# Kernel tuning notes

Measured on AMD Instinct MI355X. Metric: run time of the kernel, lower is better.

Reference implementation:

```python
import jax, jax.numpy as jnp
import numpy as np

N = 50000      # nodes
E = 500000     # edges
F_IN = 128     # num_features
H = 128        # hidden_dim
G = 256        # graphs in batch


def setup_inputs() -> dict:
    key = jax.random.key(0)
    ks = jax.random.split(key, 12)
    x = jax.random.normal(ks[0], (N, F_IN), jnp.float32)
    edge_index = jax.random.randint(ks[1], (2, E), 0, N, dtype=jnp.int32)
    edge_attr = jax.random.uniform(ks[2], (E,), jnp.float32)  # positive edge weights
    batch = jnp.sort(jax.random.randint(ks[3], (N,), 0, G, dtype=jnp.int32))
    s_in = 1.0 / np.sqrt(F_IN)
    s_h = 1.0 / np.sqrt(H)
    return {
        "x": x,
        "edge_index": edge_index,
        "edge_attr": edge_attr,
        "batch": batch,
        "W1": jax.random.normal(ks[4], (H, F_IN), jnp.float32) * s_in,
        "b1": jnp.zeros((H,), jnp.float32),
        "W2": jax.random.normal(ks[5], (H, H), jnp.float32) * s_h,
        "b2": jnp.zeros((H,), jnp.float32),
        "fW1": jax.random.normal(ks[6], (H, H), jnp.float32) * s_h,
        "fb1": jnp.zeros((H,), jnp.float32),
        "fW2": jax.random.normal(ks[7], (1, H), jnp.float32) * s_h,
        "fb2": jnp.zeros((1,), jnp.float32),
    }


def gcn_conv(x, src, dst, ew, W, b, n):
    """PyG GCNConv: linear transform, add self-loops (weight 1),
    symmetric deg^-1/2 normalization with edge weights, scatter-add, bias."""
    h = x @ W.T                                   # [n, H]
    loop = jnp.arange(n, dtype=src.dtype)
    s = jnp.concatenate([src, loop])
    d = jnp.concatenate([dst, loop])
    w = jnp.concatenate([ew, jnp.ones((n,), x.dtype)])
    deg = jax.ops.segment_sum(w, d, num_segments=n)  # weighted in-degree incl. self-loop
    dinv = jnp.where(deg > 0, jax.lax.rsqrt(deg), 0.0)
    norm = dinv[s] * w * dinv[d]                  # [E+n]
    msg = h[s] * norm[:, None]                    # gather + scale: [E+n, H]
    out = jax.ops.segment_sum(msg, d, num_segments=n)  # scatter-add
    return out + b


def reference(x, edge_index, edge_attr, batch, W1, b1, W2, b2, fW1, fb1, fW2, fb2):
    src, dst = edge_index[0], edge_index[1]
    h = jax.nn.relu(gcn_conv(x, src, dst, edge_attr, W1, b1, N))
    h = jax.nn.relu(gcn_conv(h, src, dst, edge_attr, W2, b2, N))
    # global_mean_pool over graph ids
    sums = jax.ops.segment_sum(h, batch, num_segments=G)            # [G, H]
    counts = jax.ops.segment_sum(jnp.ones((N,), h.dtype), batch, num_segments=G)
    pooled = sums / jnp.maximum(counts, 1.0)[:, None]
    o = jax.nn.relu(pooled @ fW1.T + fb1)
    return o @ fW2.T + fb2                                          # [G, 1]
```

## Files before the change

kernel.cpp:

```cpp
#include <hip/hip_runtime.h>
#include <hip/hip_bf16.h>


#define CAP 32
#define STRIDE 64

typedef __attribute__((ext_vector_type(8))) short short8;
typedef __attribute__((ext_vector_type(4))) float floatx4;

__device__ inline unsigned short f2bf(float f) {
    unsigned int u = __float_as_uint(f);
    u += 0x7FFF + ((u >> 16) & 1);
    return (unsigned short)(u >> 16);
}
__device__ inline float bf2f(unsigned short h) {
    return __uint_as_float(((unsigned int)h) << 16);
}

__global__ void build_csr(const int* __restrict__ src, const int* __restrict__ dst,
                          const float* __restrict__ ew,
                          int* __restrict__ cnt, int2* __restrict__ csr, int e, int n) {
    int i = blockIdx.x * blockDim.x + threadIdx.x;
    if (i < e) {
        int d = dst[i];
        int r = i & 1;
        int pos = atomicAdd(&cnt[(size_t)r * n + d], 1);
        csr[((size_t)d << 6) + (r << 5) + pos] = make_int2(src[i], __float_as_int(ew[i]));
    }
}

__global__ __launch_bounds__(256) void deg_from_csr(const int* __restrict__ cnt,
        const int2* __restrict__ csr, float* __restrict__ dinv, int n) {
    int node = blockIdx.x * 8 + (threadIdx.x >> 5);
    int lane = threadIdx.x & 31;
    float s = 0.0f;
    if (node < n) {
        int c0 = cnt[node], c1 = cnt[n + node];
        const int2* b = csr + ((size_t)node << 6);
        if (lane < c0) s += __int_as_float(b[lane].y);
        if (lane < c1) s += __int_as_float(b[CAP + lane].y);
    }
#pragma unroll
    for (int off = 16; off > 0; off >>= 1) s += __shfl_down(s, off, 32);
    if (node < n && lane == 0) dinv[node] = rsqrtf(s + 1.0f);
}

__global__ __launch_bounds__(256) void fold_dinv(const int* __restrict__ cnt,
        int2* __restrict__ csr, const float* __restrict__ dinv, int n) {
    int node = blockIdx.x * 8 + (threadIdx.x >> 5);
    if (node >= n) return;
    int lane = threadIdx.x & 31;
    int c0 = cnt[node], c1 = cnt[n + node];
    int2* b = csr + ((size_t)node << 6);
    if (lane < c0) {
        int2 e = b[lane];
        e.y = __float_as_int(__int_as_float(e.y) * dinv[e.x]);
        b[lane] = e;
    }
    if (lane < c1) {
        int2 e = b[CAP + lane];
        e.y = __float_as_int(__int_as_float(e.y) * dinv[e.x]);
        b[CAP + lane] = e;
    }
}

#define PW 136
__global__ __launch_bounds__(256) void gemm_nt_mfma(const float* __restrict__ X,
        const float* __restrict__ W, unsigned short* __restrict__ C, int M) {
    __shared__ unsigned short whi[128 * PW];
    __shared__ unsigned short wlo[128 * PW];
    const int t = threadIdx.x;

    {
        int j = t >> 1;
        int c0 = (t & 1) * 64;
        const floatx4* wr = (const floatx4*)(W + (size_t)j * 128 + c0);
        unsigned short* dh = &whi[j * PW + c0];
        unsigned short* dl = &wlo[j * PW + c0];
#pragma unroll
        for (int i = 0; i < 16; ++i) {
            floatx4 v = wr[i];
            ushort4 hv, lv;
            hv.x = f2bf(v.x); lv.x = f2bf(v.x - bf2f(hv.x));
            hv.y = f2bf(v.y); lv.y = f2bf(v.y - bf2f(hv.y));
            hv.z = f2bf(v.z); lv.z = f2bf(v.z - bf2f(hv.z));
            hv.w = f2bf(v.w); lv.w = f2bf(v.w - bf2f(hv.w));
            *(ushort4*)(dh + i * 4) = hv;
            *(ushort4*)(dl + i * 4) = lv;
        }
    }
    __syncthreads();

    const int wave = t >> 6;
    const int lane = t & 63;
    const int q = lane >> 4;
    const int ln = lane & 15;
    const int rowbase = blockIdx.x * 128 + wave * 32;

    floatx4 acc[2][8];
#pragma unroll
    for (int s = 0; s < 2; ++s)
#pragma unroll
        for (int ct = 0; ct < 8; ++ct) acc[s][ct] = (floatx4){0.f, 0.f, 0.f, 0.f};

#pragma unroll
    for (int ks = 0; ks < 4; ++ks) {
        short8 ahi[2], alo[2];
#pragma unroll
        for (int s = 0; s < 2; ++s) {
            int row = rowbase + s * 16 + ln;
            int rowc = (row < M) ? row : (M - 1);
            const floatx4* xr = (const floatx4*)(X + (size_t)rowc * 128 + ks * 32 + q * 8);
            floatx4 x0 = xr[0];
            floatx4 x1 = xr[1];
            unsigned short h, l;
            h = f2bf(x0.x); l = f2bf(x0.x - bf2f(h)); ahi[s][0] = (short)h; alo[s][0] = (short)l;
            h = f2bf(x0.y); l = f2bf(x0.y - bf2f(h)); ahi[s][1] = (short)h; alo[s][1] = (short)l;
            h = f2bf(x0.z); l = f2bf(x0.z - bf2f(h)); ahi[s][2] = (short)h; alo[s][2] = (short)l;
            h = f2bf(x0.w); l = f2bf(x0.w - bf2f(h)); ahi[s][3] = (short)h; alo[s][3] = (short)l;
            h = f2bf(x1.x); l = f2bf(x1.x - bf2f(h)); ahi[s][4] = (short)h; alo[s][4] = (short)l;
            h = f2bf(x1.y); l = f2bf(x1.y - bf2f(h)); ahi[s][5] = (short)h; alo[s][5] = (short)l;
            h = f2bf(x1.z); l = f2bf(x1.z - bf2f(h)); ahi[s][6] = (short)h; alo[s][6] = (short)l;
            h = f2bf(x1.w); l = f2bf(x1.w - bf2f(h)); ahi[s][7] = (short)h; alo[s][7] = (short)l;
        }
#pragma unroll
        for (int ct = 0; ct < 8; ++ct) {
            int lidx = (ct * 16 + ln) * PW + ks * 32 + q * 8;
            short8 bhi = *(const short8*)&whi[lidx];
            short8 blo = *(const short8*)&wlo[lidx];
#pragma unroll
            for (int s = 0; s < 2; ++s) {
                acc[s][ct] = __builtin_amdgcn_mfma_f32_16x16x32_bf16(ahi[s], bhi, acc[s][ct], 0, 0, 0);
                acc[s][ct] = __builtin_amdgcn_mfma_f32_16x16x32_bf16(ahi[s], blo, acc[s][ct], 0, 0, 0);
                acc[s][ct] = __builtin_amdgcn_mfma_f32_16x16x32_bf16(alo[s], bhi, acc[s][ct], 0, 0, 0);
            }
        }
    }

#pragma unroll
    for (int s = 0; s < 2; ++s) {
#pragma unroll
        for (int r = 0; r < 4; ++r) {
            int row = rowbase + s * 16 + q * 4 + r;
            if (row < M) {
                unsigned short* cr = C + (size_t)row * 128 + ln;
#pragma unroll
                for (int ct = 0; ct < 8; ++ct) cr[ct * 16] = f2bf(acc[s][ct][r]);
            }
        }
    }
}

__global__ __launch_bounds__(256) void aggregate_finalize(
        const unsigned short* __restrict__ h, const unsigned short* __restrict__ hlin,
        const int* __restrict__ cnt, const int2* __restrict__ csr,
        const float* __restrict__ dinv, const float* __restrict__ bias,
        float* __restrict__ outb, int n) {
    int node = blockIdx.x * 8 + (threadIdx.x >> 5);
    if (node >= n) return;
    int lane = threadIdx.x & 31;
    float di = dinv[node];
    float sl = di * di;
    float4 b4 = ((const float4*)bias)[lane];
    ushort4 bse = ((const ushort4*)(hlin + (size_t)node * 128))[lane];
    float4 acc = make_float4(0.f, 0.f, 0.f, 0.f);

    const int2* b = csr + ((size_t)node << 6);
    int c0 = cnt[node], c1 = cnt[n + node];
#pragma unroll
    for (int seg = 0; seg < 2; ++seg) {
        const int2* bs = b + seg * CAP;
        int c = seg ? c1 : c0;
        const int4* bv = (const int4*)bs;
        int k = 0;
        for (; k + 2 <= c; k += 2) {
            int4 e2 = bv[k >> 1];
            float w0 = __int_as_float(e2.y);
            float w1 = __int_as_float(e2.w);
            ushort4 h0 = ((const ushort4*)(h + (size_t)e2.x * 128))[lane];
            ushort4 h1 = ((const ushort4*)(h + (size_t)e2.z * 128))[lane];
            acc.x += bf2f(h0.x) * w0 + bf2f(h1.x) * w1;
            acc.y += bf2f(h0.y) * w0 + bf2f(h1.y) * w1;
            acc.z += bf2f(h0.z) * w0 + bf2f(h1.z) * w1;
            acc.w += bf2f(h0.w) * w0 + bf2f(h1.w) * w1;
        }
        if (k < c) {
            int2 ed = bs[k];
            float w = __int_as_float(ed.y);
            ushort4 hv = ((const ushort4*)(h + (size_t)ed.x * 128))[lane];
            acc.x += bf2f(hv.x) * w;
            acc.y += bf2f(hv.y) * w;
            acc.z += bf2f(hv.z) * w;
            acc.w += bf2f(hv.w) * w;
        }
    }
    float4 o;
    o.x = fmaxf(acc.x * di + bf2f(bse.x) * sl + b4.x, 0.0f);
    o.y = fmaxf(acc.y * di + bf2f(bse.y) * sl + b4.y, 0.0f);
    o.z = fmaxf(acc.z * di + bf2f(bse.z) * sl + b4.z, 0.0f);
    o.w = fmaxf(acc.w * di + bf2f(bse.w) * sl + b4.w, 0.0f);
    ((float4*)(outb + (size_t)node * 128))[lane] = o;
}

#define POOL_BLOCKS 1024
__global__ __launch_bounds__(128) void pool_partial(const float* __restrict__ h,
        const int* __restrict__ batch, float* __restrict__ pooled, int n) {
    int chunk = (n + POOL_BLOCKS - 1) / POOL_BLOCKS;
    int s = blockIdx.x * chunk;
    if (s >= n) return;
    int e = min(s + chunk, n);
    int j = threadIdx.x;
    int curg = batch[s];
    float sum = 0.0f;
    for (int i = s; i < e; ++i) {
        int g = batch[i];
        if (g != curg) {
            atomicAdd(&pooled[(size_t)curg * 128 + j], sum);
            sum = 0.0f;
            curg = g;
        }
        sum += h[(size_t)i * 128 + j];
    }
    atomicAdd(&pooled[(size_t)curg * 128 + j], sum);
}

__global__ __launch_bounds__(128) void head_mlp(const float* __restrict__ pooled,
        const int* __restrict__ batch, int n,
        const float* __restrict__ fW1, const float* __restrict__ fb1,
        const float* __restrict__ fW2, const float* __restrict__ fb2,
        float* __restrict__ out) {
    int g = blockIdx.x;
    int j = threadIdx.x;
    int lo = 0, hi = n;
    while (lo < hi) { int mid = (lo + hi) >> 1; if (batch[mid] < g) lo = mid + 1; else hi = mid; }
    int s = lo;
    hi = n;
    while (lo < hi) { int mid = (lo + hi) >> 1; if (batch[mid] < g + 1) lo = mid + 1; else hi = mid; }
    int cnt = lo - s;
    float scale = 1.0f / fmaxf((float)cnt, 1.0f);

    __shared__ float row[128];
    __shared__ float part[2];
    row[j] = pooled[(size_t)g * 128 + j] * scale;
    __syncthreads();
    float acc = fb1[j];
    const float* wr = fW1 + (size_t)j * 128;
#pragma unroll 8
    for (int k = 0; k < 128; ++k) acc += row[k] * wr[k];
    float v = fmaxf(acc, 0.0f) * fW2[j];
#pragma unroll
    for (int off = 32; off > 0; off >>= 1) v += __shfl_down(v, off);
    if ((j & 63) == 0) part[j >> 6] = v;
    __syncthreads();
    if (j == 0) out[g] = part[0] + part[1] + fb2[0];
}

extern "C" void kernel_launch(void* const* d_in, const int* in_sizes, int n_in,
                              void* d_out, int out_size, void* d_ws, size_t ws_size,
                              hipStream_t stream) {
    const float* x   = (const float*)d_in[0];
    const int*   ei  = (const int*)d_in[1];
    const float* ew  = (const float*)d_in[2];
    const int* batch = (const int*)d_in[3];
    const float* W1  = (const float*)d_in[4];
    const float* b1  = (const float*)d_in[5];
    const float* W2  = (const float*)d_in[6];
    const float* b2  = (const float*)d_in[7];
    const float* fW1 = (const float*)d_in[8];
    const float* fb1 = (const float*)d_in[9];
    const float* fW2 = (const float*)d_in[10];
    const float* fb2 = (const float*)d_in[11];
    float* out = (float*)d_out;

    const int N = in_sizes[0] / 128;
    const int E = in_sizes[2];
    const int G = out_size;
    const int* src = ei;
    const int* dst = ei + E;

    unsigned short* A = (unsigned short*)d_ws;
    float* B    = (float*)(A + (size_t)N * 128);
    int2*  csr  = (int2*)(B + (size_t)N * 128);
    int*   cnt  = (int*)(csr + (size_t)N * STRIDE);
    float* dinv = (float*)(cnt + (size_t)2 * N);
    float* pooled = dinv + N;

    hipMemsetAsync(cnt, 0, (size_t)2 * N * sizeof(int), stream);
    build_csr<<<(E + 255) / 256, 256, 0, stream>>>(src, dst, ew, cnt, csr, E, N);
    deg_from_csr<<<(N + 7) / 8, 256, 0, stream>>>(cnt, csr, dinv, N);
    fold_dinv<<<(N + 7) / 8, 256, 0, stream>>>(cnt, csr, dinv, N);

    gemm_nt_mfma<<<(N + 127) / 128, 256, 0, stream>>>(x, W1, A, N);
    aggregate_finalize<<<(N + 7) / 8, 256, 0, stream>>>(A, A, cnt, csr, dinv, b1, B, N);

    gemm_nt_mfma<<<(N + 127) / 128, 256, 0, stream>>>(B, W2, A, N);
    aggregate_finalize<<<(N + 7) / 8, 256, 0, stream>>>(A, A, cnt, csr, dinv, b2, B, N);

    hipMemsetAsync(pooled, 0, (size_t)G * 128 * sizeof(float), stream);
    pool_partial<<<POOL_BLOCKS, 128, 0, stream>>>(B, batch, pooled, N);
    head_mlp<<<G, 128, 0, stream>>>(pooled, batch, N, fW1, fb1, fW2, fb2, out);
}
```

Before: 244.8 us.

## Use four CSR count replicas, compact per-node edge lists, unroll aggregation by four

Edges are binned into four per-node sub-buckets of 16 slots instead of two of 32, which spreads the atomic counter traffic in CSR construction. The dinv-folding pass now also compacts the four sub-buckets into one contiguous list and writes the total count. The aggregation kernel then walks a single list with a 4-way unrolled gather, aiming for more loads in flight and less segment-loop overhead. The cost is extra index arithmetic in the fold pass, and each sub-bucket now overflows above 16 edges instead of 32.

```diff
diff --git a/kernel.cpp b/kernel.cpp
--- a/kernel.cpp
+++ b/kernel.cpp
@@ -2,7 +2,8 @@
 #include <hip/hip_bf16.h>
 
 
-#define CAP 32
+#define CAP 16
+#define NREP 4
 #define STRIDE 64
 
 typedef __attribute__((ext_vector_type(8))) short short8;
@@ -23,9 +24,9 @@
     int i = blockIdx.x * blockDim.x + threadIdx.x;
     if (i < e) {
         int d = dst[i];
-        int r = i & 1;
+        int r = i & (NREP - 1);
         int pos = atomicAdd(&cnt[(size_t)r * n + d], 1);
-        csr[((size_t)d << 6) + (r << 5) + pos] = make_int2(src[i], __float_as_int(ew[i]));
+        csr[((size_t)d << 6) + (r << 4) + pos] = make_int2(src[i], __float_as_int(ew[i]));
     }
 }
 
@@ -35,33 +36,45 @@
     int lane = threadIdx.x & 31;
     float s = 0.0f;
     if (node < n) {
-        int c0 = cnt[node], c1 = cnt[n + node];
+        int pos = lane & 15;
+        int sa = lane >> 4;
+        int sb = 2 + (lane >> 4);
+        int ca = cnt[(size_t)sa * n + node];
+        int cb = cnt[(size_t)sb * n + node];
         const int2* b = csr + ((size_t)node << 6);
-        if (lane < c0) s += __int_as_float(b[lane].y);
-        if (lane < c1) s += __int_as_float(b[CAP + lane].y);
+        if (pos < ca) s += __int_as_float(b[lane].y);
+        if (pos < cb) s += __int_as_float(b[32 + lane].y);
     }
 #pragma unroll
     for (int off = 16; off > 0; off >>= 1) s += __shfl_down(s, off, 32);
     if (node < n && lane == 0) dinv[node] = rsqrtf(s + 1.0f);
 }
 
-__global__ __launch_bounds__(256) void fold_dinv(const int* __restrict__ cnt,
+__global__ __launch_bounds__(256) void fold_compact(int* __restrict__ cnt,
         int2* __restrict__ csr, const float* __restrict__ dinv, int n) {
     int node = blockIdx.x * 8 + (threadIdx.x >> 5);
     if (node >= n) return;
     int lane = threadIdx.x & 31;
-    int c0 = cnt[node], c1 = cnt[n + node];
+    int c0 = cnt[node];
+    int c1 = cnt[(size_t)1 * n + node];
+    int c2 = cnt[(size_t)2 * n + node];
+    int c3 = cnt[(size_t)3 * n + node];
+    int pre[4] = {0, c0, c0 + c1, c0 + c1 + c2};
+    int cs[4] = {c0, c1, c2, c3};
+
     int2* b = csr + ((size_t)node << 6);
-    if (lane < c0) {
-        int2 e = b[lane];
-        e.y = __float_as_int(__int_as_float(e.y) * dinv[e.x]);
-        b[lane] = e;
-    }
-    if (lane < c1) {
-        int2 e = b[CAP + lane];
-        e.y = __float_as_int(__int_as_float(e.y) * dinv[e.x]);
-        b[CAP + lane] = e;
-    }
+    int pos = lane & 15;
+    int sa = lane >> 4;
+    int sb = 2 + (lane >> 4);
+    bool va = pos < cs[sa];
+    bool vb = pos < cs[sb];
+    int2 ea = va ? b[lane] : make_int2(0, 0);
+    int2 eb = vb ? b[32 + lane] : make_int2(0, 0);
+    if (va) ea.y = __float_as_int(__int_as_float(ea.y) * dinv[ea.x]);
+    if (vb) eb.y = __float_as_int(__int_as_float(eb.y) * dinv[eb.x]);
+    if (va) b[pre[sa] + pos] = ea;
+    if (vb) b[pre[sb] + pos] = eb;
+    if (lane == 0) cnt[node] = c0 + c1 + c2 + c3;
 }
 
 #define PW 136
@@ -166,33 +179,45 @@
     float4 acc = make_float4(0.f, 0.f, 0.f, 0.f);
 
     const int2* b = csr + ((size_t)node << 6);
-    int c0 = cnt[node], c1 = cnt[n + node];
-#pragma unroll
-    for (int seg = 0; seg < 2; ++seg) {
-        const int2* bs = b + seg * CAP;
-        int c = seg ? c1 : c0;
-        const int4* bv = (const int4*)bs;
-        int k = 0;
-        for (; k + 2 <= c; k += 2) {
-            int4 e2 = bv[k >> 1];
-            float w0 = __int_as_float(e2.y);
-            float w1 = __int_as_float(e2.w);
-            ushort4 h0 = ((const ushort4*)(h + (size_t)e2.x * 128))[lane];
-            ushort4 h1 = ((const ushort4*)(h + (size_t)e2.z * 128))[lane];
-            acc.x += bf2f(h0.x) * w0 + bf2f(h1.x) * w1;
-            acc.y += bf2f(h0.y) * w0 + bf2f(h1.y) * w1;
-            acc.z += bf2f(h0.z) * w0 + bf2f(h1.z) * w1;
-            acc.w += bf2f(h0.w) * w0 + bf2f(h1.w) * w1;
-        }
-        if (k < c) {
-            int2 ed = bs[k];
-            float w = __int_as_float(ed.y);
-            ushort4 hv = ((const ushort4*)(h + (size_t)ed.x * 128))[lane];
-            acc.x += bf2f(hv.x) * w;
-            acc.y += bf2f(hv.y) * w;
-            acc.z += bf2f(hv.z) * w;
-            acc.w += bf2f(hv.w) * w;
-        }
+    const int4* bv = (const int4*)b;
+    int c = cnt[node];
+    int k = 0;
+    for (; k + 4 <= c; k += 4) {
+        int4 ea = bv[k >> 1];
+        int4 eb = bv[(k >> 1) + 1];
+        float w0 = __int_as_float(ea.y);
+        float w1 = __int_as_float(ea.w);
+        float w2 = __int_as_float(eb.y);
+        float w3 = __int_as_float(eb.w);
+        ushort4 h0 = ((const ushort4*)(h + (size_t)ea.x * 128))[lane];
+        ushort4 h1 = ((const ushort4*)(h + (size_t)ea.z * 128))[lane];
+        ushort4 h2 = ((const ushort4*)(h + (size_t)eb.x * 128))[lane];
+        ushort4 h3 = ((const ushort4*)(h + (size_t)eb.z * 128))[lane];
+        acc.x += bf2f(h0.x) * w0 + bf2f(h1.x) * w1 + bf2f(h2.x) * w2 + bf2f(h3.x) * w3;
+        acc.y += bf2f(h0.y) * w0 + bf2f(h1.y) * w1 + bf2f(h2.y) * w2 + bf2f(h3.y) * w3;
+        acc.z += bf2f(h0.z) * w0 + bf2f(h1.z) * w1 + bf2f(h2.z) * w2 + bf2f(h3.z) * w3;
+        acc.w += bf2f(h0.w) * w0 + bf2f(h1.w) * w1 + bf2f(h2.w) * w2 + bf2f(h3.w) * w3;
+    }
+    if (k + 2 <= c) {
+        int4 ea = bv[k >> 1];
+        float w0 = __int_as_float(ea.y);
+        float w1 = __int_as_float(ea.w);
+        ushort4 h0 = ((const ushort4*)(h + (size_t)ea.x * 128))[lane];
+        ushort4 h1 = ((const ushort4*)(h + (size_t)ea.z * 128))[lane];
+        acc.x += bf2f(h0.x) * w0 + bf2f(h1.x) * w1;
+        acc.y += bf2f(h0.y) * w0 + bf2f(h1.y) * w1;
+        acc.z += bf2f(h0.z) * w0 + bf2f(h1.z) * w1;
+        acc.w += bf2f(h0.w) * w0 + bf2f(h1.w) * w1;
+        k += 2;
+    }
+    if (k < c) {
+        int2 ed = b[k];
+        float w = __int_as_float(ed.y);
+        ushort4 hv = ((const ushort4*)(h + (size_t)ed.x * 128))[lane];
+        acc.x += bf2f(hv.x) * w;
+        acc.y += bf2f(hv.y) * w;
+        acc.z += bf2f(hv.z) * w;
+        acc.w += bf2f(hv.w) * w;
     }
     float4 o;
     o.x = fmaxf(acc.x * di + bf2f(bse.x) * sl + b4.x, 0.0f);
@@ -282,13 +307,13 @@
     float* B    = (float*)(A + (size_t)N * 128);
     int2*  csr  = (int2*)(B + (size_t)N * 128);
     int*   cnt  = (int*)(csr + (size_t)N * STRIDE);
-    float* dinv = (float*)(cnt + (size_t)2 * N);
+    float* dinv = (float*)(cnt + (size_t)NREP * N);
     float* pooled = dinv + N;
 
-    hipMemsetAsync(cnt, 0, (size_t)2 * N * sizeof(int), stream);
+    hipMemsetAsync(cnt, 0, (size_t)NREP * N * sizeof(int), stream);
     build_csr<<<(E + 255) / 256, 256, 0, stream>>>(src, dst, ew, cnt, csr, E, N);
     deg_from_csr<<<(N + 7) / 8, 256, 0, stream>>>(cnt, csr, dinv, N);
-    fold_dinv<<<(N + 7) / 8, 256, 0, stream>>>(cnt, csr, dinv, N);
+    fold_compact<<<(N + 7) / 8, 256, 0, stream>>>(cnt, csr, dinv, N);
 
     gemm_nt_mfma<<<(N + 127) / 128, 256, 0, stream>>>(x, W1, A, N);
     aggregate_finalize<<<(N + 7) / 8, 256, 0, stream>>>(A, A, cnt, csr, dinv, b1, B, N);
```

Result: no change. 243.7 us (-0.5%).
